# Kernel tuning notes

Hardware: AMD Instinct MI355X
Metric: run time of the kernel (lower is better)

## Reference

```python
import jax, jax.numpy as jnp
import numpy as np
import math

THRESHOLD = 0.9
CAPACITY_FACTOR = 1.0
ALPHA = 0.01


def setup_inputs() -> dict:
    key = jax.random.key(0)
    k1, k2 = jax.random.split(key)
    B, T, H, E = 8, 4096, 1024, 64
    x = jax.random.normal(k1, (B, T, H), dtype=jnp.float32)
    # kaiming-uniform-ish gate init: bound = 1/sqrt(H)
    gate_w = jax.random.uniform(k2, (E, H), dtype=jnp.float32,
                                minval=-1.0 / math.sqrt(H), maxval=1.0 / math.sqrt(H))
    return {"x": x, "gate_w": gate_w}


def reference(x, gate_w):
    B, T, H = x.shape
    E = gate_w.shape[0]
    N = B * T
    x_flat = x.reshape(N, H)

    logits = x_flat @ gate_w.T                      # [N, E]
    probs = jax.nn.softmax(logits, axis=-1)

    # per-token descending sort of expert probs
    idx_sorted = jnp.argsort(-probs, axis=-1)       # [N, E]
    p_sorted = jnp.take_along_axis(probs, idx_sorted, axis=-1)

    # variable-k threshold selection on cumulative prob
    csum = jnp.cumsum(p_sorted, axis=-1)
    reached = csum >= THRESHOLD
    reached = reached.at[:, -1].set(True)
    k_idx = jnp.argmax(reached, axis=-1)            # first True per row
    arangeE = jnp.arange(E)[None, :]
    assign_sorted = arangeE <= k_idx[:, None]       # prefix-select in sorted order

    # scatter back to expert order via inverse permutation
    inv_perm = jnp.argsort(idx_sorted, axis=-1)
    assign_mask = jnp.take_along_axis(assign_sorted, inv_perm, axis=-1)

    # priority score R: prob minus rank, -1e9 for unassigned
    rank = jnp.arange(1, E + 1, dtype=probs.dtype)[None, :]
    R_sorted = jnp.where(assign_sorted, p_sorted - rank, jnp.float32(-1e9))
    R = jnp.take_along_axis(R_sorted, inv_perm, axis=-1)  # [N, E]

    # capacity-based dropping: keep top-C tokens per expert column
    capacity = int(math.ceil(N / E) * CAPACITY_FACTOR)
    C = min(capacity, N)
    tok_sorted = jnp.argsort(-R, axis=0)            # [N, E]
    topC_tok = tok_sorted[:C, :]                    # [C, E]
    cols = jnp.broadcast_to(jnp.arange(E)[None, :], topC_tok.shape)
    keep_flags = jnp.zeros((N, E), dtype=bool).at[topC_tok, cols].set(True)

    final_mask = assign_mask & keep_flags
    scores_sel = jnp.where(final_mask, probs, jnp.zeros_like(probs))

    # aux load-balance loss on top-1 assignments
    top1_idx = jnp.argmax(probs, axis=-1)
    top1_scores = jnp.max(probs, axis=-1)
    fi = jnp.mean(jax.nn.one_hot(top1_idx, E, dtype=probs.dtype), axis=0)
    pi = jax.ops.segment_sum(top1_scores, top1_idx, num_segments=E) / jnp.float32(N)
    aux_loss = E * jnp.sum(fi * pi) * ALPHA

    return final_mask, scores_sel, aux_loss, top1_idx
```

## Files before the change

kernel.cpp:

```cpp
#include <hip/hip_runtime.h>
#include <math.h>

#define NTOK 32768
#define HDIM 1024
#define NEXP 64
#define NE   (NTOK * NEXP)
#define CAP  512
#define TB   32
#define CK   64
#define XRS  68
#define CAND 6144
#define QMAX 2048

__device__ __forceinline__ unsigned f2key(float f) {
  unsigned u = __float_as_uint(f);
  return (u & 0x80000000u) ? ~u : (u | 0x80000000u);
}
__device__ __forceinline__ int bin_of(unsigned k) {
  if (k & 0x80000000u) return 0;
  float f = __uint_as_float(~k);
  f = fminf(f, 64.5f);
  return (int)f;
}

__global__ void init_kernel(unsigned* cnt, float* sumP, unsigned* ghist) {
  int i = blockIdx.x * 256 + threadIdx.x;
  if (i < NEXP) { cnt[i] = 0u; sumP[i] = 0.f; }
  if (i < NEXP * NEXP) ghist[i] = 0u;
}

__global__ __launch_bounds__(256) void router_kernel(
    const float* __restrict__ x, const float* __restrict__ w,
    float* __restrict__ probs, unsigned* __restrict__ keyNE,
    unsigned* __restrict__ keyEN, unsigned long long* __restrict__ assignB,
    unsigned* __restrict__ cnt, float* __restrict__ sumP,
    unsigned* __restrict__ ghist, float* __restrict__ out) {
  __shared__ float sm[(TB + NEXP) * XRS];
  __shared__ unsigned lhist[NEXP * 17];
  const int tid  = threadIdx.x;
  const int wid  = tid >> 6, lane = tid & 63;
  const int tokv = wid >> 1, expv = wid & 1;
  const int tg   = lane >> 3, eg = lane & 7;
  const int t0   = blockIdx.x * TB;
  float* xs  = sm;
  float* wsm = sm + TB * XRS;

  for (int i = tid; i < NEXP * 17; i += 256) lhist[i] = 0u;

  float acc[2][4] = {};

  for (int hc = 0; hc < HDIM / CK; ++hc) {
    const int h0 = hc * CK;
#pragma unroll
    for (int r = 0; r < 2; ++r) {
      int idx = tid + r * 256;
      int row = idx >> 4, c4 = idx & 15;
      *(float4*)(xs + row * XRS + c4 * 4) =
          *(const float4*)(x + (size_t)(t0 + row) * HDIM + h0 + c4 * 4);
    }
#pragma unroll
    for (int r = 0; r < 4; ++r) {
      int idx = tid + r * 256;
      int row = idx >> 4, c4 = idx & 15;
      *(float4*)(wsm + row * XRS + c4 * 4) =
          *(const float4*)(w + (size_t)row * HDIM + h0 + c4 * 4);
    }
    __syncthreads();
#pragma unroll
    for (int s = 0; s < 16; ++s) {
      const int k4 = s * 4;
      float4 xv0 = *(const float4*)(xs + (tokv * 16 + tg) * XRS + k4);
      float4 xv1 = *(const float4*)(xs + (tokv * 16 + 8 + tg) * XRS + k4);
#pragma unroll
      for (int j = 0; j < 4; ++j) {
        float4 wv = *(const float4*)(wsm + (expv * 32 + j * 8 + eg) * XRS + k4);
        acc[0][j] += xv0.x * wv.x + xv0.y * wv.y + xv0.z * wv.z + xv0.w * wv.w;
        acc[1][j] += xv1.x * wv.x + xv1.y * wv.y + xv1.z * wv.z + xv1.w * wv.w;
      }
    }
    __syncthreads();
  }

  float* ls = sm;
  unsigned* kt = (unsigned*)(sm + TB * 65);
#pragma unroll
  for (int i = 0; i < 2; ++i) {
    int tl = tokv * 16 + i * 8 + tg;
#pragma unroll
    for (int j = 0; j < 4; ++j)
      ls[tl * 65 + expv * 32 + j * 8 + eg] = acc[i][j];
  }
  __syncthreads();

  for (int i = 0; i < 8; ++i) {
    const int tl = wid * 8 + i;
    const int t  = t0 + tl;
    float l = ls[tl * 65 + lane];
    float mx = l;
#pragma unroll
    for (int m = 32; m >= 1; m >>= 1) mx = fmaxf(mx, __shfl_xor(mx, m));
    float ex = expf(l - mx);
    float ssum = ex;
#pragma unroll
    for (int m = 32; m >= 1; m >>= 1) ssum += __shfl_xor(ssum, m);
    float p = ex / ssum;
    int rank = 0; float csum = p;
#pragma unroll
    for (int d = 1; d < 64; ++d) {
      float pj = __shfl_xor(p, d);
      int H = d; H |= H >> 1; H |= H >> 2; H |= H >> 4; H -= (H >> 1);
      bool jlt = (lane & H) != 0;
      bool gt = (pj > p) || (pj == p && jlt);
      rank += gt ? 1 : 0;
      csum += gt ? pj : 0.f;
    }
    int kc = (csum >= 0.9f) ? rank : 63;
#pragma unroll
    for (int m = 32; m >= 1; m >>= 1) kc = min(kc, __shfl_xor(kc, m));
    const bool assign = (rank <= kc);
    float R = assign ? (p - (float)(rank + 1)) : -1e9f;
    unsigned key = f2key(R);
    probs[(size_t)t * NEXP + lane] = p;
    keyNE[(size_t)t * NEXP + lane] = key;
    kt[tl * 65 + lane] = key;
    {
      int b = bin_of(key);
      atomicAdd(&lhist[lane * 17 + (b >> 2)], 1u << ((b & 3) * 8));
    }
    unsigned long long ab = __ballot(assign);
    if (lane == 0) assignB[t] = ab;
    if (rank == 0) {
      out[(size_t)2 * NE + 1 + t] = (float)lane;
      atomicAdd(&cnt[lane], 1u);
      atomicAdd(&sumP[lane], p);
    }
  }
  __syncthreads();
#pragma unroll
  for (int r = 0; r < 8; ++r) {
    int idx = tid + r * 256;
    int e = idx >> 5, tl = idx & 31;
    keyEN[(size_t)e * NTOK + t0 + tl] = kt[tl * 65 + e];
  }
  for (int idx = tid; idx < NEXP * NEXP; idx += 256) {
    int ee = idx >> 6, b = idx & 63;
    unsigned v = (lhist[ee * 17 + (b >> 2)] >> ((b & 3) * 8)) & 0xffu;
    if (v) atomicAdd(&ghist[idx], v);
  }
}

__global__ __launch_bounds__(1024) void select_kernel(
    const unsigned* __restrict__ keyEN, const unsigned* __restrict__ ghist,
    unsigned* __restrict__ theta, int* __restrict__ tieCut) {
  const int e = blockIdx.x;
  const unsigned* col = keyEN + (size_t)e * NTOK;
  const int tid = threadIdx.x, wid = tid >> 6;
  __shared__ unsigned wh[16][256];
  __shared__ unsigned h[256];
  __shared__ unsigned cA_k[CAND], cA_t[CAND], cB_k[CAND], cB_t[CAND];
  __shared__ unsigned s_n, s_b;
  __shared__ int s_rb, s_need, s_cnt;
  __shared__ unsigned s_theta; __shared__ int s_cut;

  if (tid == 0) {
    unsigned run = 0; int rb = -1, need = 0, cc = 0;
    for (int r = 0; r < 64; ++r) {
      unsigned c = ghist[e * 64 + r];
      if (rb < 0 && run + c >= CAP) { rb = r; need = CAP - (int)run; cc = (int)c; }
      run += c;
    }
    s_rb = rb; s_need = need; s_cnt = cc;
  }
  __syncthreads();
  if (s_rb < 0) {
    if (tid == 0) { theta[e] = f2key(-1e9f); tieCut[e] = -1; }
    return;
  }
  const int rb = s_rb;
  int need = s_need, cnt = s_cnt;
  unsigned pmask = 0u, pval = 0u;
  int level = 0;

  while (cnt > CAND && level < 4) {
    const int sh = 24 - 8 * level;
    for (int r = tid; r < 16 * 256; r += 1024) ((unsigned*)wh)[r] = 0u;
    __syncthreads();
    for (int t = tid; t < NTOK; t += 1024) {
      unsigned k = col[t];
      if (bin_of(k) == rb && (k & pmask) == pval)
        atomicAdd(&wh[wid][(k >> sh) & 255u], 1u);
    }
    __syncthreads();
    if (tid < 256) {
      unsigned s = 0;
      for (int wv = 0; wv < 16; ++wv) s += wh[wv][tid];
      h[tid] = s;
    }
    __syncthreads();
    if (tid == 0) {
      unsigned cum = 0;
      for (int d = 255; d >= 0; --d) {
        if (cum + h[d] >= (unsigned)need) {
          s_b = (unsigned)d; s_need = need - (int)cum; s_cnt = (int)h[d];
          break;
        }
        cum += h[d];
      }
    }
    __syncthreads();
    need = s_need; cnt = s_cnt;
    pmask |= (255u << sh); pval |= (s_b << sh);
    level++;
    __syncthreads();
  }

  if (cnt > CAND) {
    int lo = 0, hi = NTOK - 1;
    while (lo < hi) {
      int mid = (lo + hi) >> 1;
      if (tid == 0) s_n = 0u;
      __syncthreads();
      for (int t = tid; t <= mid; t += 1024)
        if (col[t] == pval) atomicAdd(&s_n, 1u);
      __syncthreads();
      if ((int)s_n >= need) hi = mid; else lo = mid + 1;
      __syncthreads();
    }
    if (tid == 0) { theta[e] = pval; tieCut[e] = lo; }
    return;
  }

  if (tid == 0) s_n = 0u;
  __syncthreads();
  for (int t = tid; t < NTOK; t += 1024) {
    unsigned k = col[t];
    if (bin_of(k) == rb && (k & pmask) == pval) {
      unsigned i = atomicAdd(&s_n, 1u);
      cA_k[i] = k; cA_t[i] = (unsigned)t;
    }
  }
  __syncthreads();
  unsigned* ck = cA_k; unsigned* ct = cA_t;
  unsigned* nk = cB_k; unsigned* nt2 = cB_t;

  while (cnt > QMAX && level < 4) {
    const int sh = 24 - 8 * level;
    for (int r = tid; r < 16 * 256; r += 1024) ((unsigned*)wh)[r] = 0u;
    __syncthreads();
    for (int i = tid; i < cnt; i += 1024)
      atomicAdd(&wh[wid][(ck[i] >> sh) & 255u], 1u);
    __syncthreads();
    if (tid < 256) {
      unsigned s = 0;
      for (int wv = 0; wv < 16; ++wv) s += wh[wv][tid];
      h[tid] = s;
    }
    __syncthreads();
    if (tid == 0) {
      unsigned cum = 0;
      for (int d = 255; d >= 0; --d) {
        if (cum + h[d] >= (unsigned)need) {
          s_b = (unsigned)d; s_need = need - (int)cum; s_cnt = (int)h[d];
          break;
        }
        cum += h[d];
      }
      s_n = 0u;
    }
    __syncthreads();
    for (int i = tid; i < cnt; i += 1024) {
      if (((ck[i] >> sh) & 255u) == s_b) {
        unsigned j = atomicAdd(&s_n, 1u);
        nk[j] = ck[i]; nt2[j] = ct[i];
      }
    }
    __syncthreads();
    { unsigned* t1 = ck; ck = nk; nk = t1; t1 = ct; ct = nt2; nt2 = t1; }
    need = s_need; cnt = s_cnt; level++;
    __syncthreads();
  }

  for (int i = tid; i < cnt; i += 1024) {
    unsigned ki = ck[i], ti = ct[i];
    int c = 0;
    for (int j = 0; j < cnt; ++j) {
      unsigned kj = ck[j], tj = ct[j];
      c += (kj > ki || (kj == ki && tj < ti)) ? 1 : 0;
    }
    if (c == need - 1) { s_theta = ki; s_cut = (int)ti; }
  }
  __syncthreads();
  if (tid == 0) { theta[e] = s_theta; tieCut[e] = s_cut; }
}

__global__ __launch_bounds__(256) void write_kernel(
    const float* __restrict__ probs, const unsigned* __restrict__ keyNE,
    const unsigned long long* __restrict__ assignB,
    const unsigned* __restrict__ theta, const int* __restrict__ tieCut,
    const unsigned* __restrict__ cnt, const float* __restrict__ sumP,
    float* __restrict__ out) {
  const int id = blockIdx.x * 256 + threadIdx.x;
  const int t = id >> 6, e = id & 63;
  unsigned k = keyNE[id];
  float p = probs[id];
  bool a = (assignB[t] >> e) & 1ull;
  unsigned th = theta[e];
  int cut = tieCut[e];
  bool keep = (k > th) || ((k == th) && (t <= cut));
  bool msk = a && keep;
  out[id] = msk ? 1.f : 0.f;
  out[(size_t)NE + id] = msk ? p : 0.f;
  if (blockIdx.x == 0 && threadIdx.x < 64) {
    int ee = threadIdx.x;
    float v = ((float)cnt[ee] / (float)NTOK) * (sumP[ee] / (float)NTOK);
#pragma unroll
    for (int m = 32; m >= 1; m >>= 1) v += __shfl_xor(v, m);
    if (ee == 0) out[(size_t)2 * NE] = (float)NEXP * v * 0.01f;
  }
}

extern "C" void kernel_launch(void* const* d_in, const int* in_sizes, int n_in,
                              void* d_out, int out_size, void* d_ws, size_t ws_size,
                              hipStream_t stream) {
  const float* x = (const float*)d_in[0];
  const float* w = (const float*)d_in[1];
  float* out = (float*)d_out;

  char* ws = (char*)d_ws;
  float* probs                 = (float*)ws;
  unsigned* keyNE              = (unsigned*)(probs + NE);
  unsigned* keyEN              = keyNE + NE;
  unsigned long long* assignB  = (unsigned long long*)(keyEN + NE);
  unsigned* cnt                = (unsigned*)(assignB + NTOK);
  float* sumP                  = (float*)(cnt + NEXP);
  unsigned* theta              = (unsigned*)(sumP + NEXP);
  int* tieCut                  = (int*)(theta + NEXP);
  unsigned* ghist              = (unsigned*)(tieCut + NEXP);

  init_kernel<<<16, 256, 0, stream>>>(cnt, sumP, ghist);
  router_kernel<<<NTOK / TB, 256, 0, stream>>>(x, w, probs, keyNE, keyEN,
                                               assignB, cnt, sumP, ghist, out);
  select_kernel<<<NEXP, 1024, 0, stream>>>(keyEN, ghist, theta, tieCut);
  write_kernel<<<NE / 256, 256, 0, stream>>>(probs, keyNE, assignB, theta,
                                             tieCut, cnt, sumP, out);
}
```

Before: 540.8 us.

## Double router token tile to 64 and use 4x4 register blocking

```diff
diff --git a/kernel.cpp b/kernel.cpp
--- a/kernel.cpp
+++ b/kernel.cpp
@@ -6,7 +6,7 @@
 #define NEXP 64
 #define NE   (NTOK * NEXP)
 #define CAP  512
-#define TB   32
+#define TB   64
 #define CK   64
 #define XRS  68
 #define CAND 6144
@@ -39,29 +39,24 @@
   __shared__ unsigned lhist[NEXP * 17];
   const int tid  = threadIdx.x;
   const int wid  = tid >> 6, lane = tid & 63;
-  const int tokv = wid >> 1, expv = wid & 1;
-  const int tg   = lane >> 3, eg = lane & 7;
+  const int tg   = lane >> 4;
+  const int eg   = lane & 15;
   const int t0   = blockIdx.x * TB;
   float* xs  = sm;
   float* wsm = sm + TB * XRS;
 
   for (int i = tid; i < NEXP * 17; i += 256) lhist[i] = 0u;
 
-  float acc[2][4] = {};
+  float acc[4][4] = {};
 
   for (int hc = 0; hc < HDIM / CK; ++hc) {
     const int h0 = hc * CK;
 #pragma unroll
-    for (int r = 0; r < 2; ++r) {
+    for (int r = 0; r < 4; ++r) {
       int idx = tid + r * 256;
       int row = idx >> 4, c4 = idx & 15;
       *(float4*)(xs + row * XRS + c4 * 4) =
           *(const float4*)(x + (size_t)(t0 + row) * HDIM + h0 + c4 * 4);
-    }
-#pragma unroll
-    for (int r = 0; r < 4; ++r) {
-      int idx = tid + r * 256;
-      int row = idx >> 4, c4 = idx & 15;
       *(float4*)(wsm + row * XRS + c4 * 4) =
           *(const float4*)(w + (size_t)row * HDIM + h0 + c4 * 4);
     }
@@ -69,14 +64,19 @@
 #pragma unroll
     for (int s = 0; s < 16; ++s) {
       const int k4 = s * 4;
-      float4 xv0 = *(const float4*)(xs + (tokv * 16 + tg) * XRS + k4);
-      float4 xv1 = *(const float4*)(xs + (tokv * 16 + 8 + tg) * XRS + k4);
-#pragma unroll
-      for (int j = 0; j < 4; ++j) {
-        float4 wv = *(const float4*)(wsm + (expv * 32 + j * 8 + eg) * XRS + k4);
-        acc[0][j] += xv0.x * wv.x + xv0.y * wv.y + xv0.z * wv.z + xv0.w * wv.w;
-        acc[1][j] += xv1.x * wv.x + xv1.y * wv.y + xv1.z * wv.z + xv1.w * wv.w;
-      }
+      float4 xv[4], wv[4];
+#pragma unroll
+      for (int i = 0; i < 4; ++i)
+        xv[i] = *(const float4*)(xs + (wid * 16 + i * 4 + tg) * XRS + k4);
+#pragma unroll
+      for (int j = 0; j < 4; ++j)
+        wv[j] = *(const float4*)(wsm + (j * 16 + eg) * XRS + k4);
+#pragma unroll
+      for (int i = 0; i < 4; ++i)
+#pragma unroll
+        for (int j = 0; j < 4; ++j)
+          acc[i][j] += xv[i].x * wv[j].x + xv[i].y * wv[j].y +
+                       xv[i].z * wv[j].z + xv[i].w * wv[j].w;
     }
     __syncthreads();
   }
@@ -84,16 +84,16 @@
   float* ls = sm;
   unsigned* kt = (unsigned*)(sm + TB * 65);
 #pragma unroll
-  for (int i = 0; i < 2; ++i) {
-    int tl = tokv * 16 + i * 8 + tg;
+  for (int i = 0; i < 4; ++i) {
+    int tl = wid * 16 + i * 4 + tg;
 #pragma unroll
     for (int j = 0; j < 4; ++j)
-      ls[tl * 65 + expv * 32 + j * 8 + eg] = acc[i][j];
-  }
-  __syncthreads();
-
-  for (int i = 0; i < 8; ++i) {
-    const int tl = wid * 8 + i;
+      ls[tl * 65 + j * 16 + eg] = acc[i][j];
+  }
+  __syncthreads();
+
+  for (int i = 0; i < 16; ++i) {
+    const int tl = wid * 16 + i;
     const int t  = t0 + tl;
     float l = ls[tl * 65 + lane];
     float mx = l;
@@ -137,9 +137,9 @@
   }
   __syncthreads();
 #pragma unroll
-  for (int r = 0; r < 8; ++r) {
+  for (int r = 0; r < 16; ++r) {
     int idx = tid + r * 256;
-    int e = idx >> 5, tl = idx & 31;
+    int e = idx >> 6, tl = idx & 63;
     keyEN[(size_t)e * NTOK + t0 + tl] = kt[tl * 65 + e];
   }
   for (int idx = tid; idx < NEXP * NEXP; idx += 256) {
```

Result: slower. 576.1 us (+6.5%).
